# Performance work log

Measured on AMD Instinct MI355X. Metric: run time of the kernel, lower is better.

## Reference

```python
import jax, jax.numpy as jnp
import numpy as np

K_TOP = 8
TEMP = 0.1


def setup_inputs() -> dict:
    key = jax.random.key(0)
    k1, k2, k3, k4 = jax.random.split(key, 4)
    B, K, D, Db, C = 256, 64, 256, 512, 1024
    return {
        "slot_features": jax.random.normal(k1, (B, K, D), dtype=jnp.float32),
        "proj_W": jax.random.normal(k2, (D, Db), dtype=jnp.float32) * (1.0 / np.sqrt(D)),
        "proj_b": jax.random.normal(k3, (Db,), dtype=jnp.float32) * 0.01,
        "embed": jax.random.uniform(k4, (C, Db), dtype=jnp.float32),  # NMF atoms are nonnegative
    }


def reference(slot_features, proj_W, proj_b, embed):
    B, K, _ = slot_features.shape
    num_codes = embed.shape[0]

    # slot projection: [B, K, basis_dim]
    z_e = jnp.einsum('bkd,de->bke', slot_features, proj_W) + proj_b
    z_flat = z_e.reshape(B * K, -1)  # [N, Db]

    # Euclidean cdist via expanded squared norm (the GEMM is the heavy part)
    d2 = (jnp.sum(z_flat * z_flat, axis=-1, keepdims=True)
          + jnp.sum(embed * embed, axis=-1)[None, :]
          - 2.0 * (z_flat @ embed.T))  # [N, C]
    dist = jnp.sqrt(jnp.maximum(d2, 0.0))

    # top-k smallest distances
    neg_vals, indices_flat = jax.lax.top_k(-dist, K_TOP)  # [N, k]
    values = -neg_vals
    weights = jax.nn.softmax(-values / TEMP, axis=-1)  # [N, k]

    # gather atoms and interpolate
    selected_atoms = embed[indices_flat]  # [N, k, Db]
    q_flat = jnp.einsum('nk,nkd->nd', weights, selected_atoms)
    q_st = q_flat.reshape(B, K, -1)

    vq_loss = jnp.mean((z_e - jax.lax.stop_gradient(q_st)) ** 2)

    # average usage (equivalent to scatter into [N, C] then mean over N)
    avg_usage = jax.ops.segment_sum(weights.reshape(-1), indices_flat.reshape(-1),
                                    num_segments=num_codes) / (B * K)
    entropy = -jnp.sum(avg_usage * jnp.log(avg_usage + 1e-8))

    indices = indices_flat[:, 0].reshape(B, K)
    return q_st, indices, vq_loss, entropy
```

## Files before the change

### kernel.cpp

```cpp
#include <hip/hip_runtime.h>
#include <math.h>
#include <float.h>

#define NROWS  16384
#define DIN    256
#define DBASIS 512
#define CCODES 1024
#define KTOP   8
#define NCAND  16
#define TEMP_F 0.1f

typedef __attribute__((ext_vector_type(8))) short short8v;
typedef __attribute__((ext_vector_type(4))) float f32x4;

__device__ __forceinline__ unsigned short bf16_rne(float f) {
    unsigned int u = __float_as_uint(f);
    u += 0x7FFFu + ((u >> 16) & 1u);
    return (unsigned short)(u >> 16);
}
__device__ __forceinline__ float bf16_to_f32(unsigned short h) {
    return __uint_as_float(((unsigned int)h) << 16);
}

__global__ __launch_bounds__(256) void k_prep(const float* __restrict__ embed,
                                              unsigned short* __restrict__ Eh,
                                              unsigned short* __restrict__ El,
                                              float* __restrict__ en2,
                                              float* __restrict__ usage,
                                              float* __restrict__ vq_accum) {
    const int c = blockIdx.x * 256 + threadIdx.x;
    const float4* row = (const float4*)(embed + (size_t)c * DBASIS);
    ushort4* ehr = (ushort4*)(Eh + (size_t)c * DBASIS);
    ushort4* elr = (ushort4*)(El + (size_t)c * DBASIS);
    float s = 0.f;
    #pragma unroll 4
    for (int j = 0; j < DBASIS / 4; ++j) {
        const float4 v = row[j];
        s += v.x * v.x + v.y * v.y + v.z * v.z + v.w * v.w;
        ushort4 h, l;
        h.x = bf16_rne(v.x); l.x = bf16_rne(v.x - bf16_to_f32(h.x));
        h.y = bf16_rne(v.y); l.y = bf16_rne(v.y - bf16_to_f32(h.y));
        h.z = bf16_rne(v.z); l.z = bf16_rne(v.z - bf16_to_f32(h.z));
        h.w = bf16_rne(v.w); l.w = bf16_rne(v.w - bf16_to_f32(h.w));
        ehr[j] = h; elr[j] = l;
    }
    en2[c] = s;
    usage[c] = 0.f;
    if (c == 0) vq_accum[0] = 0.f;
}

__global__ __launch_bounds__(256, 2) void k_gemm_z(const float* __restrict__ A,
                                                   const float* __restrict__ Bm,
                                                   const float* __restrict__ bias,
                                                   float* __restrict__ Z,
                                                   unsigned short* __restrict__ Zh,
                                                   unsigned short* __restrict__ Zl) {
    __shared__ float As[16][132];
    __shared__ float Bs[16][132];
    const int tid = threadIdx.x;
    const int bm = blockIdx.x * 128;
    const int bn = blockIdx.y * 128;
    const int tx = tid & 15, ty = tid >> 4;
    float acc[2][2][4][4] = {};

    for (int k0 = 0; k0 < DIN; k0 += 16) {
        #pragma unroll
        for (int it = 0; it < 2; ++it) {
            const int r  = (tid >> 2) + it * 64;
            const int c4 = (tid & 3) * 4;
            const float4 a = *(const float4*)(A + (size_t)(bm + r) * DIN + k0 + c4);
            As[c4 + 0][r] = a.x; As[c4 + 1][r] = a.y;
            As[c4 + 2][r] = a.z; As[c4 + 3][r] = a.w;
        }
        {
            const int r  = tid >> 4;
            const int c8 = (tid & 15) * 8;
            const float4 b0 = *(const float4*)(Bm + (size_t)(k0 + r) * DBASIS + bn + c8);
            const float4 b1 = *(const float4*)(Bm + (size_t)(k0 + r) * DBASIS + bn + c8 + 4);
            *(float4*)&Bs[r][c8]     = b0;
            *(float4*)&Bs[r][c8 + 4] = b1;
        }
        __syncthreads();
        #pragma unroll
        for (int kk = 0; kk < 16; ++kk) {
            const float4 a0 = *(const float4*)&As[kk][ty * 4];
            const float4 a1 = *(const float4*)&As[kk][64 + ty * 4];
            const float4 b0 = *(const float4*)&Bs[kk][tx * 4];
            const float4 b1 = *(const float4*)&Bs[kk][64 + tx * 4];
            const float av[2][4] = {{a0.x, a0.y, a0.z, a0.w}, {a1.x, a1.y, a1.z, a1.w}};
            const float bv[2][4] = {{b0.x, b0.y, b0.z, b0.w}, {b1.x, b1.y, b1.z, b1.w}};
            #pragma unroll
            for (int qi = 0; qi < 2; ++qi)
                #pragma unroll
                for (int qj = 0; qj < 2; ++qj)
                    #pragma unroll
                    for (int i = 0; i < 4; ++i)
                        #pragma unroll
                        for (int j = 0; j < 4; ++j)
                            acc[qi][qj][i][j] = fmaf(av[qi][i], bv[qj][j], acc[qi][qj][i][j]);
        }
        __syncthreads();
    }
    #pragma unroll
    for (int qj = 0; qj < 2; ++qj) {
        const int colb = bn + qj * 64 + tx * 4;
        const float4 bv = *(const float4*)(bias + colb);
        const float bb[4] = {bv.x, bv.y, bv.z, bv.w};
        #pragma unroll
        for (int qi = 0; qi < 2; ++qi)
            #pragma unroll
            for (int i = 0; i < 4; ++i) {
                const int row = bm + qi * 64 + ty * 4 + i;
                float4 o;
                o.x = acc[qi][qj][i][0] + bb[0];
                o.y = acc[qi][qj][i][1] + bb[1];
                o.z = acc[qi][qj][i][2] + bb[2];
                o.w = acc[qi][qj][i][3] + bb[3];
                *(float4*)(Z + (size_t)row * DBASIS + colb) = o;
                ushort4 h, l;
                h.x = bf16_rne(o.x); l.x = bf16_rne(o.x - bf16_to_f32(h.x));
                h.y = bf16_rne(o.y); l.y = bf16_rne(o.y - bf16_to_f32(h.y));
                h.z = bf16_rne(o.z); l.z = bf16_rne(o.z - bf16_to_f32(h.z));
                h.w = bf16_rne(o.w); l.w = bf16_rne(o.w - bf16_to_f32(h.w));
                *(ushort4*)(Zh + (size_t)row * DBASIS + colb) = h;
                *(ushort4*)(Zl + (size_t)row * DBASIS + colb) = l;
            }
    }
}

__global__ __launch_bounds__(256, 2) void k_gemm_p(const unsigned short* __restrict__ Zh,
                                                   const unsigned short* __restrict__ Zl,
                                                   const unsigned short* __restrict__ Eh,
                                                   const unsigned short* __restrict__ El,
                                                   const float* __restrict__ en2,
                                                   float* __restrict__ P) {
    __shared__ __align__(16) short ldsA[4096];
    __shared__ __align__(16) short ldsB[4096];
    const int tid  = threadIdx.x;
    const int lane = tid & 63;
    const int w    = tid >> 6;
    const int wr   = w >> 1, wc = w & 1;
    const int bm   = blockIdx.x * 128;
    const int bc   = blockIdx.y * 128;

    f32x4 acc[4][4];
    #pragma unroll
    for (int i = 0; i < 4; ++i)
        #pragma unroll
        for (int j = 0; j < 4; ++j)
            acc[i][j] = (f32x4){0.f, 0.f, 0.f, 0.f};

    for (int ch = 0; ch < 48; ++ch) {
        const int term = ch >> 4;
        const int k0   = (ch & 15) * 32;
        const unsigned short* Asrc = (term == 2) ? Zl : Zh;
        const unsigned short* Bsrc = (term == 1) ? El : Eh;
        #pragma unroll
        for (int j = 0; j < 2; ++j) {
            const int gi = j * 256 + tid;
            const int g  = gi >> 7;
            const int r  = gi & 127;
            const unsigned short* ga = Asrc + (size_t)(bm + r) * DBASIS + k0 + g * 8;
            const unsigned short* gb = Bsrc + (size_t)(bc + r) * DBASIS + k0 + g * 8;
            __builtin_amdgcn_global_load_lds((const __attribute__((address_space(1))) void*)ga,
                                             (__attribute__((address_space(3))) void*)(&ldsA[gi * 8]),
                                             16, 0, 0);
            __builtin_amdgcn_global_load_lds((const __attribute__((address_space(1))) void*)gb,
                                             (__attribute__((address_space(3))) void*)(&ldsB[gi * 8]),
                                             16, 0, 0);
        }
        __syncthreads();

        const int kg = lane >> 4;
        const int lr = lane & 15;
        short8v af[4], bf[4];
        #pragma unroll
        for (int f = 0; f < 4; ++f) {
            af[f] = *(const short8v*)&ldsA[(kg * 128 + wr * 64 + f * 16 + lr) * 8];
            bf[f] = *(const short8v*)&ldsB[(kg * 128 + wc * 64 + f * 16 + lr) * 8];
        }
        #pragma unroll
        for (int fm = 0; fm < 4; ++fm)
            #pragma unroll
            for (int fn = 0; fn < 4; ++fn)
                acc[fm][fn] = __builtin_amdgcn_mfma_f32_16x16x32_bf16(af[fm], bf[fn], acc[fm][fn], 0, 0, 0);
        __syncthreads();
    }

    #pragma unroll
    for (int fn = 0; fn < 4; ++fn) {
        const int col = bc + wc * 64 + fn * 16 + (lane & 15);
        const float e2 = en2[col];
        #pragma unroll
        for (int fm = 0; fm < 4; ++fm) {
            const int row0 = bm + wr * 64 + fm * 16 + (lane >> 4) * 4;
            #pragma unroll
            for (int r = 0; r < 4; ++r)
                P[(size_t)(row0 + r) * CCODES + col] = e2 - 2.f * acc[fm][fn][r];
        }
    }
}

__global__ __launch_bounds__(256) void k_topk(const float* __restrict__ P,
                                              const float* __restrict__ Z,
                                              const float* __restrict__ embed,
                                              const float* __restrict__ en2,
                                              float* __restrict__ q_out,
                                              float* __restrict__ idx_out,
                                              float* __restrict__ usage,
                                              float* __restrict__ vq_accum) {
    const int tid  = threadIdx.x;
    const int lane = tid & 63;
    const int w    = tid >> 6;
    const int n    = blockIdx.x * 4 + w;

    float v[16];
    #pragma unroll
    for (int j = 0; j < 16; ++j) v[j] = P[(size_t)n * CCODES + lane + 64 * j];

    float zv[8];
    float zn2 = 0.f;
    #pragma unroll
    for (int j = 0; j < 8; ++j) {
        zv[j] = Z[(size_t)n * DBASIS + lane + 64 * j];
        zn2 = fmaf(zv[j], zv[j], zn2);
    }
    #pragma unroll
    for (int off = 32; off; off >>= 1) zn2 += __shfl_xor(zn2, off, 64);

    int idx16[NCAND];
    #pragma unroll
    for (int t = 0; t < NCAND; ++t) {
        float bv = v[0];
        int   bj = 0;
        #pragma unroll
        for (int j = 1; j < 16; ++j)
            if (v[j] < bv) { bv = v[j]; bj = j; }
        int bcn = lane + 64 * bj;
        #pragma unroll
        for (int off = 32; off; off >>= 1) {
            const float ov = __shfl_xor(bv, off, 64);
            const int   oc = __shfl_xor(bcn, off, 64);
            if (ov < bv || (ov == bv && oc < bcn)) { bv = ov; bcn = oc; }
        }
        idx16[t] = bcn;
        const int kl = bcn & 63, kj = bcn >> 6;
        #pragma unroll
        for (int j = 0; j < 16; ++j)
            if (lane == kl && j == kj) v[j] = FLT_MAX;
    }

    float d16[NCAND];
    #pragma unroll
    for (int t = 0; t < NCAND; ++t) {
        const int c = idx16[t];
        const float* er = embed + (size_t)c * DBASIS;
        float dot = 0.f;
        #pragma unroll
        for (int j = 0; j < 8; ++j) dot = fmaf(zv[j], er[lane + 64 * j], dot);
        #pragma unroll
        for (int off = 32; off; off >>= 1) dot += __shfl_xor(dot, off, 64);
        const float d2 = zn2 + en2[c] - 2.f * dot;
        d16[t] = sqrtf(fmaxf(d2, 0.f));
    }

    float dist[KTOP];
    int   idx[KTOP];
    #pragma unroll
    for (int t = 0; t < KTOP; ++t) {
        float bd = d16[0];
        int   bi = idx16[0];
        int   bu = 0;
        #pragma unroll
        for (int u = 1; u < NCAND; ++u) {
            const bool better = (d16[u] < bd) || (d16[u] == bd && idx16[u] < bi);
            if (better) { bd = d16[u]; bi = idx16[u]; bu = u; }
        }
        dist[t] = bd; idx[t] = bi;
        #pragma unroll
        for (int u = 0; u < NCAND; ++u)
            if (u == bu) d16[u] = FLT_MAX;
    }

    float wgt[KTOP];
    float s = 0.f;
    #pragma unroll
    for (int t = 0; t < KTOP; ++t) {
        wgt[t] = expf((dist[0] - dist[t]) * (1.0f / TEMP_F));
        s += wgt[t];
    }
    const float inv_s = 1.f / s;
    #pragma unroll
    for (int t = 0; t < KTOP; ++t) wgt[t] *= inv_s;

    float lloss = 0.f;
    #pragma unroll
    for (int j = 0; j < 8; ++j) {
        const int d = lane + 64 * j;
        float acc = 0.f;
        #pragma unroll
        for (int t = 0; t < KTOP; ++t)
            acc = fmaf(wgt[t], embed[(size_t)idx[t] * DBASIS + d], acc);
        q_out[(size_t)n * DBASIS + d] = acc;
        const float df = zv[j] - acc;
        lloss = fmaf(df, df, lloss);
    }
    #pragma unroll
    for (int off = 32; off; off >>= 1) lloss += __shfl_xor(lloss, off, 64);

    __shared__ float ls[4];
    if (lane == 0) ls[w] = lloss;
    __syncthreads();
    if (tid == 0) atomicAdd(vq_accum, ls[0] + ls[1] + ls[2] + ls[3]);

    #pragma unroll
    for (int t = 0; t < KTOP; ++t)
        if (lane == t) atomicAdd(usage + idx[t], wgt[t] * (1.0f / (float)NROWS));

    if (lane == 0) idx_out[n] = (float)idx[0];
}

__global__ __launch_bounds__(256) void k_final(const float* __restrict__ usage,
                                               const float* __restrict__ vq_accum,
                                               float* __restrict__ out_scalars) {
    __shared__ float red[256];
    float s = 0.f;
    for (int c = threadIdx.x; c < CCODES; c += 256) {
        const float u = usage[c];
        s += u * logf(u + 1e-8f);
    }
    red[threadIdx.x] = s;
    __syncthreads();
    for (int st = 128; st; st >>= 1) {
        if (threadIdx.x < st) red[threadIdx.x] += red[threadIdx.x + st];
        __syncthreads();
    }
    if (threadIdx.x == 0) {
        out_scalars[0] = vq_accum[0] * (1.0f / ((float)NROWS * (float)DBASIS));
        out_scalars[1] = -red[0];
    }
}

extern "C" void kernel_launch(void* const* d_in, const int* in_sizes, int n_in,
                              void* d_out, int out_size, void* d_ws, size_t ws_size,
                              hipStream_t stream) {
    const float* slot  = (const float*)d_in[0];
    const float* projW = (const float*)d_in[1];
    const float* projb = (const float*)d_in[2];
    const float* embed = (const float*)d_in[3];

    float* out  = (float*)d_out;
    float* q    = out;
    float* idxo = out + (size_t)NROWS * DBASIS;
    float* scal = idxo + NROWS;

    char* wsb = (char*)d_ws;
    float*          Z     = (float*)wsb;                                  wsb += (size_t)NROWS * DBASIS * 4;
    float*          P     = (float*)wsb;                                  wsb += (size_t)NROWS * CCODES * 4;
    unsigned short* Zh    = (unsigned short*)wsb;                         wsb += (size_t)NROWS * DBASIS * 2;
    unsigned short* Zl    = (unsigned short*)wsb;                         wsb += (size_t)NROWS * DBASIS * 2;
    unsigned short* Eh    = (unsigned short*)wsb;                         wsb += (size_t)CCODES * DBASIS * 2;
    unsigned short* El    = (unsigned short*)wsb;                         wsb += (size_t)CCODES * DBASIS * 2;
    float*          en2   = (float*)wsb;                                  wsb += CCODES * 4;
    float*          usage = (float*)wsb;                                  wsb += CCODES * 4;
    float*          vq    = (float*)wsb;

    k_prep<<<dim3(CCODES / 256), dim3(256), 0, stream>>>(embed, Eh, El, en2, usage, vq);
    k_gemm_z<<<dim3(NROWS / 128, DBASIS / 128), dim3(256), 0, stream>>>(slot, projW, projb, Z, Zh, Zl);
    k_gemm_p<<<dim3(NROWS / 128, CCODES / 128), dim3(256), 0, stream>>>(Zh, Zl, Eh, El, en2, P);
    k_topk<<<dim3(NROWS / 4), dim3(256), 0, stream>>>(P, Z, embed, en2, q, idxo, usage, vq);
    k_final<<<dim3(1), dim3(256), 0, stream>>>(usage, vq, scal);
}
```

Before: 411.1 us.

## Move projection GEMM to split-bf16 MFMA and use ballot threshold top-k selection

Replaces the fp32 SIMT projection GEMM with a three-term bf16 MFMA GEMM (hi*hi, hi*lo, lo*hi). Two new prep kernels split the slot features and the transposed weights into high and low bf16 parts. The top-k kernel now packs distance and code index into a 32-bit key. A ballot-driven binary search finds a threshold that admits at least 16 candidates, which are compacted into LDS and rescored exactly in fp32. This drops the 16 serial wave-wide argmin passes but adds extra prep traffic and a data-dependent number of candidates to rescore.

```diff
diff --git a/kernel.cpp b/kernel.cpp
--- a/kernel.cpp
+++ b/kernel.cpp
@@ -7,7 +7,6 @@
 #define DBASIS 512
 #define CCODES 1024
 #define KTOP   8
-#define NCAND  16
 #define TEMP_F 0.1f
 
 typedef __attribute__((ext_vector_type(8))) short short8v;
@@ -20,6 +19,10 @@
 }
 __device__ __forceinline__ float bf16_to_f32(unsigned short h) {
     return __uint_as_float(((unsigned int)h) << 16);
+}
+__device__ __forceinline__ unsigned packkey(float p, float zn2, unsigned cidx) {
+    const float d2 = fmaxf(p + zn2, 0.f);
+    return (__float_as_uint(d2) & 0xFFFFFC00u) | cidx;
 }
 
 __global__ __launch_bounds__(256) void k_prep(const float* __restrict__ embed,
@@ -49,82 +52,119 @@
     if (c == 0) vq_accum[0] = 0.f;
 }
 
-__global__ __launch_bounds__(256, 2) void k_gemm_z(const float* __restrict__ A,
-                                                   const float* __restrict__ Bm,
-                                                   const float* __restrict__ bias,
-                                                   float* __restrict__ Z,
-                                                   unsigned short* __restrict__ Zh,
-                                                   unsigned short* __restrict__ Zl) {
-    __shared__ float As[16][132];
-    __shared__ float Bs[16][132];
-    const int tid = threadIdx.x;
-    const int bm = blockIdx.x * 128;
-    const int bn = blockIdx.y * 128;
-    const int tx = tid & 15, ty = tid >> 4;
-    float acc[2][2][4][4] = {};
-
-    for (int k0 = 0; k0 < DIN; k0 += 16) {
-        #pragma unroll
-        for (int it = 0; it < 2; ++it) {
-            const int r  = (tid >> 2) + it * 64;
-            const int c4 = (tid & 3) * 4;
-            const float4 a = *(const float4*)(A + (size_t)(bm + r) * DIN + k0 + c4);
-            As[c4 + 0][r] = a.x; As[c4 + 1][r] = a.y;
-            As[c4 + 2][r] = a.z; As[c4 + 3][r] = a.w;
-        }
-        {
-            const int r  = tid >> 4;
-            const int c8 = (tid & 15) * 8;
-            const float4 b0 = *(const float4*)(Bm + (size_t)(k0 + r) * DBASIS + bn + c8);
-            const float4 b1 = *(const float4*)(Bm + (size_t)(k0 + r) * DBASIS + bn + c8 + 4);
-            *(float4*)&Bs[r][c8]     = b0;
-            *(float4*)&Bs[r][c8 + 4] = b1;
+__global__ __launch_bounds__(256) void k_prep_slot(const float* __restrict__ in,
+                                                   unsigned short* __restrict__ Sh,
+                                                   unsigned short* __restrict__ Sl) {
+    const int i = blockIdx.x * 256 + threadIdx.x;
+    const float4 v = ((const float4*)in)[i];
+    ushort4 h, l;
+    h.x = bf16_rne(v.x); l.x = bf16_rne(v.x - bf16_to_f32(h.x));
+    h.y = bf16_rne(v.y); l.y = bf16_rne(v.y - bf16_to_f32(h.y));
+    h.z = bf16_rne(v.z); l.z = bf16_rne(v.z - bf16_to_f32(h.z));
+    h.w = bf16_rne(v.w); l.w = bf16_rne(v.w - bf16_to_f32(h.w));
+    ((ushort4*)Sh)[i] = h;
+    ((ushort4*)Sl)[i] = l;
+}
+
+__global__ __launch_bounds__(256) void k_prep_w(const float* __restrict__ W,
+                                                unsigned short* __restrict__ Wh,
+                                                unsigned short* __restrict__ Wl) {
+    __shared__ float tile[32][33];
+    const int k0 = blockIdx.x * 32;
+    const int n0 = blockIdx.y * 32;
+    const int tx = threadIdx.x & 31, ty = threadIdx.x >> 5;
+    #pragma unroll
+    for (int i = 0; i < 32; i += 8)
+        tile[ty + i][tx] = W[(size_t)(k0 + ty + i) * DBASIS + n0 + tx];
+    __syncthreads();
+    #pragma unroll
+    for (int i = 0; i < 32; i += 8) {
+        const int n = n0 + ty + i, k = k0 + tx;
+        const float v = tile[tx][ty + i];
+        const unsigned short h = bf16_rne(v);
+        Wh[(size_t)n * DIN + k] = h;
+        Wl[(size_t)n * DIN + k] = bf16_rne(v - bf16_to_f32(h));
+    }
+}
+
+__global__ __launch_bounds__(256, 2) void k_gemm_z_mfma(const unsigned short* __restrict__ Sh,
+                                                        const unsigned short* __restrict__ Sl,
+                                                        const unsigned short* __restrict__ Wh,
+                                                        const unsigned short* __restrict__ Wl,
+                                                        const float* __restrict__ bias,
+                                                        float* __restrict__ Z,
+                                                        unsigned short* __restrict__ Zh,
+                                                        unsigned short* __restrict__ Zl) {
+    __shared__ __align__(16) short ldsA[4096];
+    __shared__ __align__(16) short ldsB[4096];
+    const int tid  = threadIdx.x;
+    const int lane = tid & 63;
+    const int w    = tid >> 6;
+    const int wr   = w >> 1, wc = w & 1;
+    const int bm   = blockIdx.x * 128;
+    const int bc   = blockIdx.y * 128;
+
+    f32x4 acc[4][4];
+    #pragma unroll
+    for (int i = 0; i < 4; ++i)
+        #pragma unroll
+        for (int j = 0; j < 4; ++j)
+            acc[i][j] = (f32x4){0.f, 0.f, 0.f, 0.f};
+
+    for (int ch = 0; ch < 24; ++ch) {
+        const int term = ch >> 3;
+        const int k0   = (ch & 7) * 32;
+        const unsigned short* Asrc = (term == 2) ? Sl : Sh;
+        const unsigned short* Bsrc = (term == 1) ? Wl : Wh;
+        #pragma unroll
+        for (int j = 0; j < 2; ++j) {
+            const int gi = j * 256 + tid;
+            const int g  = gi >> 7;
+            const int r  = gi & 127;
+            const unsigned short* ga = Asrc + (size_t)(bm + r) * DIN + k0 + g * 8;
+            const unsigned short* gb = Bsrc + (size_t)(bc + r) * DIN + k0 + g * 8;
+            __builtin_amdgcn_global_load_lds((const __attribute__((address_space(1))) void*)ga,
+                                             (__attribute__((address_space(3))) void*)(&ldsA[gi * 8]),
+                                             16, 0, 0);
+            __builtin_amdgcn_global_load_lds((const __attribute__((address_space(1))) void*)gb,
+                                             (__attribute__((address_space(3))) void*)(&ldsB[gi * 8]),
+                                             16, 0, 0);
         }
         __syncthreads();
-        #pragma unroll
-        for (int kk = 0; kk < 16; ++kk) {
-            const float4 a0 = *(const float4*)&As[kk][ty * 4];
-            const float4 a1 = *(const float4*)&As[kk][64 + ty * 4];
-            const float4 b0 = *(const float4*)&Bs[kk][tx * 4];
-            const float4 b1 = *(const float4*)&Bs[kk][64 + tx * 4];
-            const float av[2][4] = {{a0.x, a0.y, a0.z, a0.w}, {a1.x, a1.y, a1.z, a1.w}};
-            const float bv[2][4] = {{b0.x, b0.y, b0.z, b0.w}, {b1.x, b1.y, b1.z, b1.w}};
+
+        const int kg = lane >> 4;
+        const int lr = lane & 15;
+        short8v af[4], bf[4];
+        #pragma unroll
+        for (int f = 0; f < 4; ++f) {
+            af[f] = *(const short8v*)&ldsA[(kg * 128 + wr * 64 + f * 16 + lr) * 8];
+            bf[f] = *(const short8v*)&ldsB[(kg * 128 + wc * 64 + f * 16 + lr) * 8];
+        }
+        #pragma unroll
+        for (int fm = 0; fm < 4; ++fm)
             #pragma unroll
-            for (int qi = 0; qi < 2; ++qi)
-                #pragma unroll
-                for (int qj = 0; qj < 2; ++qj)
-                    #pragma unroll
-                    for (int i = 0; i < 4; ++i)
-                        #pragma unroll
-                        for (int j = 0; j < 4; ++j)
-                            acc[qi][qj][i][j] = fmaf(av[qi][i], bv[qj][j], acc[qi][qj][i][j]);
-        }
+            for (int fn = 0; fn < 4; ++fn)
+                acc[fm][fn] = __builtin_amdgcn_mfma_f32_16x16x32_bf16(af[fm], bf[fn], acc[fm][fn], 0, 0, 0);
         __syncthreads();
     }
-    #pragma unroll
-    for (int qj = 0; qj < 2; ++qj) {
-        const int colb = bn + qj * 64 + tx * 4;
-        const float4 bv = *(const float4*)(bias + colb);
-        const float bb[4] = {bv.x, bv.y, bv.z, bv.w};
-        #pragma unroll
-        for (int qi = 0; qi < 2; ++qi)
+
+    #pragma unroll
+    for (int fn = 0; fn < 4; ++fn) {
+        const int col = bc + wc * 64 + fn * 16 + (lane & 15);
+        const float bb = bias[col];
+        #pragma unroll
+        for (int fm = 0; fm < 4; ++fm) {
+            const int row0 = bm + wr * 64 + fm * 16 + (lane >> 4) * 4;
             #pragma unroll
-            for (int i = 0; i < 4; ++i) {
-                const int row = bm + qi * 64 + ty * 4 + i;
-                float4 o;
-                o.x = acc[qi][qj][i][0] + bb[0];
-                o.y = acc[qi][qj][i][1] + bb[1];
-                o.z = acc[qi][qj][i][2] + bb[2];
-                o.w = acc[qi][qj][i][3] + bb[3];
-                *(float4*)(Z + (size_t)row * DBASIS + colb) = o;
-                ushort4 h, l;
-                h.x = bf16_rne(o.x); l.x = bf16_rne(o.x - bf16_to_f32(h.x));
-                h.y = bf16_rne(o.y); l.y = bf16_rne(o.y - bf16_to_f32(h.y));
-                h.z = bf16_rne(o.z); l.z = bf16_rne(o.z - bf16_to_f32(h.z));
-                h.w = bf16_rne(o.w); l.w = bf16_rne(o.w - bf16_to_f32(h.w));
-                *(ushort4*)(Zh + (size_t)row * DBASIS + colb) = h;
-                *(ushort4*)(Zl + (size_t)row * DBASIS + colb) = l;
+            for (int r = 0; r < 4; ++r) {
+                const float val = acc[fm][fn][r] + bb;
+                const size_t o = (size_t)(row0 + r) * DBASIS + col;
+                Z[o] = val;
+                const unsigned short h = bf16_rne(val);
+                Zh[o] = h;
+                Zl[o] = bf16_rne(val - bf16_to_f32(h));
             }
+        }
     }
 }
 
@@ -214,9 +254,8 @@
     const int w    = tid >> 6;
     const int n    = blockIdx.x * 4 + w;
 
-    float v[16];
-    #pragma unroll
-    for (int j = 0; j < 16; ++j) v[j] = P[(size_t)n * CCODES + lane + 64 * j];
+    __shared__ int   cand_lds[4][64];
+    __shared__ float ls[4];
 
     float zv[8];
     float zn2 = 0.f;
@@ -228,58 +267,70 @@
     #pragma unroll
     for (int off = 32; off; off >>= 1) zn2 += __shfl_xor(zn2, off, 64);
 
-    int idx16[NCAND];
-    #pragma unroll
-    for (int t = 0; t < NCAND; ++t) {
-        float bv = v[0];
-        int   bj = 0;
-        #pragma unroll
-        for (int j = 1; j < 16; ++j)
-            if (v[j] < bv) { bv = v[j]; bj = j; }
-        int bcn = lane + 64 * bj;
+    const float4* prow = (const float4*)(P + (size_t)n * CCODES + lane * 16);
+    const unsigned cbase = (unsigned)(lane * 16);
+    unsigned key[16];
+    #pragma unroll
+    for (int j = 0; j < 4; ++j) {
+        const float4 v = prow[j];
+        key[4 * j + 0] = packkey(v.x, zn2, cbase + 4 * j + 0);
+        key[4 * j + 1] = packkey(v.y, zn2, cbase + 4 * j + 1);
+        key[4 * j + 2] = packkey(v.z, zn2, cbase + 4 * j + 2);
+        key[4 * j + 3] = packkey(v.w, zn2, cbase + 4 * j + 3);
+    }
+
+    unsigned kmin = key[0];
+    #pragma unroll
+    for (int t = 1; t < 16; ++t) kmin = (key[t] < kmin) ? key[t] : kmin;
+
+    unsigned lo = 0u, hi = 0xFFFFFFFFu;
+    while (lo < hi) {
+        const unsigned mid = lo + ((hi - lo) >> 1);
+        const unsigned long long mk = __ballot(kmin <= mid);
+        if (__popcll(mk) >= 16) hi = mid; else lo = mid + 1;
+    }
+    const unsigned T = lo;
+
+    int* clist = cand_lds[w];
+    int base = 0;
+    #pragma unroll
+    for (int t = 0; t < 16; ++t) {
+        const bool pred = (key[t] <= T);
+        const unsigned long long mk = __ballot(pred);
+        const int pos = base + __popcll(mk & ((1ull << lane) - 1ull));
+        if (pred && pos < 64) clist[pos] = (int)(cbase + t);
+        base += __popcll(mk);
+    }
+    const int m = base < 64 ? base : 64;
+
+    float mydist = FLT_MAX;
+    int   myidx  = 0x7FFFFFFF;
+    for (int t = 0; t < m; ++t) {
+        const int c = clist[t];
+        const float* er = embed + (size_t)c * DBASIS;
+        float dot = 0.f;
+        #pragma unroll
+        for (int j = 0; j < 8; ++j) dot = fmaf(zv[j], er[lane + 64 * j], dot);
+        #pragma unroll
+        for (int off = 32; off; off >>= 1) dot += __shfl_xor(dot, off, 64);
+        const float d = sqrtf(fmaxf(zn2 + en2[c] - 2.f * dot, 0.f));
+        if (lane == t) { mydist = d; myidx = c; }
+    }
+
+    float dist[KTOP];
+    int   idx[KTOP];
+    #pragma unroll
+    for (int p = 0; p < KTOP; ++p) {
+        float bv = mydist;
+        int   bi = myidx;
         #pragma unroll
         for (int off = 32; off; off >>= 1) {
             const float ov = __shfl_xor(bv, off, 64);
-            const int   oc = __shfl_xor(bcn, off, 64);
-            if (ov < bv || (ov == bv && oc < bcn)) { bv = ov; bcn = oc; }
-        }
-        idx16[t] = bcn;
-        const int kl = bcn & 63, kj = bcn >> 6;
-        #pragma unroll
-        for (int j = 0; j < 16; ++j)
-            if (lane == kl && j == kj) v[j] = FLT_MAX;
-    }
-
-    float d16[NCAND];
-    #pragma unroll
-    for (int t = 0; t < NCAND; ++t) {
-        const int c = idx16[t];
-        const float* er = embed + (size_t)c * DBASIS;
-        float dot = 0.f;
-        #pragma unroll
-        for (int j = 0; j < 8; ++j) dot = fmaf(zv[j], er[lane + 64 * j], dot);
-        #pragma unroll
-        for (int off = 32; off; off >>= 1) dot += __shfl_xor(dot, off, 64);
-        const float d2 = zn2 + en2[c] - 2.f * dot;
-        d16[t] = sqrtf(fmaxf(d2, 0.f));
-    }
-
-    float dist[KTOP];
-    int   idx[KTOP];
-    #pragma unroll
-    for (int t = 0; t < KTOP; ++t) {
-        float bd = d16[0];
-        int   bi = idx16[0];
-        int   bu = 0;
-        #pragma unroll
-        for (int u = 1; u < NCAND; ++u) {
-            const bool better = (d16[u] < bd) || (d16[u] == bd && idx16[u] < bi);
-            if (better) { bd = d16[u]; bi = idx16[u]; bu = u; }
-        }
-        dist[t] = bd; idx[t] = bi;
-        #pragma unroll
-        for (int u = 0; u < NCAND; ++u)
-            if (u == bu) d16[u] = FLT_MAX;
+            const int   oi = __shfl_xor(bi, off, 64);
+            if (ov < bv || (ov == bv && oi < bi)) { bv = ov; bi = oi; }
+        }
+        dist[p] = bv; idx[p] = bi;
+        if (myidx == bi) { mydist = FLT_MAX; myidx = 0x7FFFFFFF; }
     }
 
     float wgt[KTOP];
@@ -308,7 +359,6 @@
     #pragma unroll
     for (int off = 32; off; off >>= 1) lloss += __shfl_xor(lloss, off, 64);
 
-    __shared__ float ls[4];
     if (lane == 0) ls[w] = lloss;
     __syncthreads();
     if (tid == 0) atomicAdd(vq_accum, ls[0] + ls[1] + ls[2] + ls[3]);
@@ -355,18 +405,24 @@
     float* scal = idxo + NROWS;
 
     char* wsb = (char*)d_ws;
-    float*          Z     = (float*)wsb;                                  wsb += (size_t)NROWS * DBASIS * 4;
-    float*          P     = (float*)wsb;                                  wsb += (size_t)NROWS * CCODES * 4;
-    unsigned short* Zh    = (unsigned short*)wsb;                         wsb += (size_t)NROWS * DBASIS * 2;
-    unsigned short* Zl    = (unsigned short*)wsb;                         wsb += (size_t)NROWS * DBASIS * 2;
-    unsigned short* Eh    = (unsigned short*)wsb;                         wsb += (size_t)CCODES * DBASIS * 2;
-    unsigned short* El    = (unsigned short*)wsb;                         wsb += (size_t)CCODES * DBASIS * 2;
-    float*          en2   = (float*)wsb;                                  wsb += CCODES * 4;
-    float*          usage = (float*)wsb;                                  wsb += CCODES * 4;
+    float*          Z     = (float*)wsb;          wsb += (size_t)NROWS * DBASIS * 4;
+    float*          P     = (float*)wsb;          wsb += (size_t)NROWS * CCODES * 4;
+    unsigned short* Zh    = (unsigned short*)wsb; wsb += (size_t)NROWS * DBASIS * 2;
+    unsigned short* Zl    = (unsigned short*)wsb; wsb += (size_t)NROWS * DBASIS * 2;
+    unsigned short* Eh    = (unsigned short*)wsb; wsb += (size_t)CCODES * DBASIS * 2;
+    unsigned short* El    = (unsigned short*)wsb; wsb += (size_t)CCODES * DBASIS * 2;
+    unsigned short* Sh    = (unsigned short*)wsb; wsb += (size_t)NROWS * DIN * 2;
+    unsigned short* Sl    = (unsigned short*)wsb; wsb += (size_t)NROWS * DIN * 2;
+    unsigned short* Wh    = (unsigned short*)wsb; wsb += (size_t)DBASIS * DIN * 2;
+    unsigned short* Wl    = (unsigned short*)wsb; wsb += (size_t)DBASIS * DIN * 2;
+    float*          en2   = (float*)wsb;          wsb += CCODES * 4;
+    float*          usage = (float*)wsb;          wsb += CCODES * 4;
     float*          vq    = (float*)wsb;
 
     k_prep<<<dim3(CCODES / 256), dim3(256), 0, stream>>>(embed, Eh, El, en2, usage, vq);
-    k_gemm_z<<<dim3(NROWS / 128, DBASIS / 128), dim3(256), 0, stream>>>(slot, projW, projb, Z, Zh, Zl);
+    k_prep_slot<<<dim3(NROWS * DIN / 4 / 256), dim3(256), 0, stream>>>(slot, Sh, Sl);
+    k_prep_w<<<dim3(DIN / 32, DBASIS / 32), dim3(256), 0, stream>>>(projW, Wh, Wl);
+    k_gemm_z_mfma<<<dim3(NROWS / 128, DBASIS / 128), dim3(256), 0, stream>>>(Sh, Sl, Wh, Wl, projb, Z, Zh, Zl);
     k_gemm_p<<<dim3(NROWS / 128, CCODES / 128), dim3(256), 0, stream>>>(Zh, Zl, Eh, El, en2, P);
     k_topk<<<dim3(NROWS / 4), dim3(256), 0, stream>>>(P, Z, embed, en2, q, idxo, usage, vq);
     k_final<<<dim3(1), dim3(256), 0, stream>>>(usage, vq, scal);
```

Result: faster. 380.6 us (-7.4%).

## Double-buffer split-bf16 GEMM and use threshold-based candidate selection in top-k

Applied to the files above, without the earlier changes.

The distance GEMM now stages all four bf16 hi/lo tiles at once into a double-buffered LDS region. It issues the three MFMA products per k-chunk, prefetching the next chunk while computing the current one, and swaps the grid axes so neighbouring blocks share Z rows. The top-k kernel replaces 16 serial wave-wide argmin passes with packed distance/index keys and a ballot-based binary search for a threshold that keeps at least 16 candidates. The candidates are compacted into LDS and exact fp32 distances are recomputed for up to 64 of them. This raises LDS usage to 64KB per block, which may reduce occupancy, and caps candidates at 64 when there are ties.

```diff
diff --git a/kernel.cpp b/kernel.cpp
--- a/kernel.cpp
+++ b/kernel.cpp
@@ -7,7 +7,6 @@
 #define DBASIS 512
 #define CCODES 1024
 #define KTOP   8
-#define NCAND  16
 #define TEMP_F 0.1f
 
 typedef __attribute__((ext_vector_type(8))) short short8v;
@@ -21,6 +20,14 @@
 __device__ __forceinline__ float bf16_to_f32(unsigned short h) {
     return __uint_as_float(((unsigned int)h) << 16);
 }
+__device__ __forceinline__ unsigned packkey(float p, float zn2, unsigned cidx) {
+    const float d2 = fmaxf(p + zn2, 0.f);
+    return (__float_as_uint(d2) & 0xFFFFFC00u) | cidx;
+}
+
+#define GLOAD16(gsrc, ldst) \
+    __builtin_amdgcn_global_load_lds((const __attribute__((address_space(1))) void*)(gsrc), \
+                                     (__attribute__((address_space(3))) void*)(ldst), 16, 0, 0)
 
 __global__ __launch_bounds__(256) void k_prep(const float* __restrict__ embed,
                                               unsigned short* __restrict__ Eh,
@@ -134,14 +141,15 @@
                                                    const unsigned short* __restrict__ El,
                                                    const float* __restrict__ en2,
                                                    float* __restrict__ P) {
-    __shared__ __align__(16) short ldsA[4096];
-    __shared__ __align__(16) short ldsB[4096];
+    __shared__ __align__(16) short lds[2][4][4096];
     const int tid  = threadIdx.x;
     const int lane = tid & 63;
     const int w    = tid >> 6;
     const int wr   = w >> 1, wc = w & 1;
-    const int bm   = blockIdx.x * 128;
-    const int bc   = blockIdx.y * 128;
+    const int bm   = blockIdx.y * 128;
+    const int bc   = blockIdx.x * 128;
+    const int kg   = lane >> 4;
+    const int lr   = lane & 15;
 
     f32x4 acc[4][4];
     #pragma unroll
@@ -150,46 +158,56 @@
         for (int j = 0; j < 4; ++j)
             acc[i][j] = (f32x4){0.f, 0.f, 0.f, 0.f};
 
-    for (int ch = 0; ch < 48; ++ch) {
-        const int term = ch >> 4;
-        const int k0   = (ch & 15) * 32;
-        const unsigned short* Asrc = (term == 2) ? Zl : Zh;
-        const unsigned short* Bsrc = (term == 1) ? El : Eh;
-        #pragma unroll
-        for (int j = 0; j < 2; ++j) {
-            const int gi = j * 256 + tid;
-            const int g  = gi >> 7;
-            const int r  = gi & 127;
-            const unsigned short* ga = Asrc + (size_t)(bm + r) * DBASIS + k0 + g * 8;
-            const unsigned short* gb = Bsrc + (size_t)(bc + r) * DBASIS + k0 + g * 8;
-            __builtin_amdgcn_global_load_lds((const __attribute__((address_space(1))) void*)ga,
-                                             (__attribute__((address_space(3))) void*)(&ldsA[gi * 8]),
-                                             16, 0, 0);
-            __builtin_amdgcn_global_load_lds((const __attribute__((address_space(1))) void*)gb,
-                                             (__attribute__((address_space(3))) void*)(&ldsB[gi * 8]),
-                                             16, 0, 0);
-        }
+#define STAGE_P(BUF, PH) do {                                                  \
+        const int k0_ = (PH) * 32;                                             \
+        _Pragma("unroll")                                                      \
+        for (int j_ = 0; j_ < 2; ++j_) {                                       \
+            const int gi_ = j_ * 256 + tid;                                    \
+            const int g_  = gi_ >> 7, r_ = gi_ & 127;                          \
+            const size_t ao_ = (size_t)(bm + r_) * DBASIS + k0_ + g_ * 8;      \
+            const size_t bo_ = (size_t)(bc + r_) * DBASIS + k0_ + g_ * 8;      \
+            GLOAD16(Zh + ao_, &lds[BUF][0][gi_ * 8]);                          \
+            GLOAD16(Zl + ao_, &lds[BUF][1][gi_ * 8]);                          \
+            GLOAD16(Eh + bo_, &lds[BUF][2][gi_ * 8]);                          \
+            GLOAD16(El + bo_, &lds[BUF][3][gi_ * 8]);                          \
+        }                                                                      \
+    } while (0)
+
+#define COMPUTE_P(BUF) do {                                                    \
+        short8v afh[4], afl[4], bfh[4], bfl[4];                                \
+        _Pragma("unroll")                                                      \
+        for (int f = 0; f < 4; ++f) {                                          \
+            const int ai = (kg * 128 + wr * 64 + f * 16 + lr) * 8;             \
+            const int bi = (kg * 128 + wc * 64 + f * 16 + lr) * 8;             \
+            afh[f] = *(const short8v*)&lds[BUF][0][ai];                        \
+            afl[f] = *(const short8v*)&lds[BUF][1][ai];                        \
+            bfh[f] = *(const short8v*)&lds[BUF][2][bi];                        \
+            bfl[f] = *(const short8v*)&lds[BUF][3][bi];                        \
+        }                                                                      \
+        _Pragma("unroll")                                                      \
+        for (int fm = 0; fm < 4; ++fm)                                         \
+            _Pragma("unroll")                                                  \
+            for (int fn = 0; fn < 4; ++fn) {                                   \
+                acc[fm][fn] = __builtin_amdgcn_mfma_f32_16x16x32_bf16(afh[fm], bfh[fn], acc[fm][fn], 0, 0, 0); \
+                acc[fm][fn] = __builtin_amdgcn_mfma_f32_16x16x32_bf16(afh[fm], bfl[fn], acc[fm][fn], 0, 0, 0); \
+                acc[fm][fn] = __builtin_amdgcn_mfma_f32_16x16x32_bf16(afl[fm], bfh[fn], acc[fm][fn], 0, 0, 0); \
+            }                                                                  \
+    } while (0)
+
+    STAGE_P(0, 0);
+    __syncthreads();
+    int cur = 0;
+    for (int ph = 0; ph < 15; ++ph) {
+        STAGE_P(cur ^ 1, ph + 1);
+        COMPUTE_P(cur);
         __syncthreads();
-
-        const int kg = lane >> 4;
-        const int lr = lane & 15;
-        short8v af[4], bf[4];
-        #pragma unroll
-        for (int f = 0; f < 4; ++f) {
-            af[f] = *(const short8v*)&ldsA[(kg * 128 + wr * 64 + f * 16 + lr) * 8];
-            bf[f] = *(const short8v*)&ldsB[(kg * 128 + wc * 64 + f * 16 + lr) * 8];
-        }
-        #pragma unroll
-        for (int fm = 0; fm < 4; ++fm)
-            #pragma unroll
-            for (int fn = 0; fn < 4; ++fn)
-                acc[fm][fn] = __builtin_amdgcn_mfma_f32_16x16x32_bf16(af[fm], bf[fn], acc[fm][fn], 0, 0, 0);
-        __syncthreads();
-    }
+        cur ^= 1;
+    }
+    COMPUTE_P(cur);
 
     #pragma unroll
     for (int fn = 0; fn < 4; ++fn) {
-        const int col = bc + wc * 64 + fn * 16 + (lane & 15);
+        const int col = bc + wc * 64 + fn * 16 + lr;
         const float e2 = en2[col];
         #pragma unroll
         for (int fm = 0; fm < 4; ++fm) {
@@ -199,6 +217,8 @@
                 P[(size_t)(row0 + r) * CCODES + col] = e2 - 2.f * acc[fm][fn][r];
         }
     }
+#undef STAGE_P
+#undef COMPUTE_P
 }
 
 __global__ __launch_bounds__(256) void k_topk(const float* __restrict__ P,
@@ -214,9 +234,8 @@
     const int w    = tid >> 6;
     const int n    = blockIdx.x * 4 + w;
 
-    float v[16];
-    #pragma unroll
-    for (int j = 0; j < 16; ++j) v[j] = P[(size_t)n * CCODES + lane + 64 * j];
+    __shared__ int   cand_lds[4][64];
+    __shared__ float ls[4];
 
     float zv[8];
     float zn2 = 0.f;
@@ -228,58 +247,70 @@
     #pragma unroll
     for (int off = 32; off; off >>= 1) zn2 += __shfl_xor(zn2, off, 64);
 
-    int idx16[NCAND];
-    #pragma unroll
-    for (int t = 0; t < NCAND; ++t) {
-        float bv = v[0];
-        int   bj = 0;
-        #pragma unroll
-        for (int j = 1; j < 16; ++j)
-            if (v[j] < bv) { bv = v[j]; bj = j; }
-        int bcn = lane + 64 * bj;
+    const float4* prow = (const float4*)(P + (size_t)n * CCODES + lane * 16);
+    const unsigned cbase = (unsigned)(lane * 16);
+    unsigned key[16];
+    #pragma unroll
+    for (int j = 0; j < 4; ++j) {
+        const float4 v = prow[j];
+        key[4 * j + 0] = packkey(v.x, zn2, cbase + 4 * j + 0);
+        key[4 * j + 1] = packkey(v.y, zn2, cbase + 4 * j + 1);
+        key[4 * j + 2] = packkey(v.z, zn2, cbase + 4 * j + 2);
+        key[4 * j + 3] = packkey(v.w, zn2, cbase + 4 * j + 3);
+    }
+
+    unsigned kmin = key[0];
+    #pragma unroll
+    for (int t = 1; t < 16; ++t) kmin = (key[t] < kmin) ? key[t] : kmin;
+
+    unsigned lo = 0u, hi = 0xFFFFFFFFu;
+    while (lo < hi) {
+        const unsigned mid = lo + ((hi - lo) >> 1);
+        const unsigned long long mk = __ballot(kmin <= mid);
+        if (__popcll(mk) >= 16) hi = mid; else lo = mid + 1;
+    }
+    const unsigned T = lo;
+
+    int* clist = cand_lds[w];
+    int base = 0;
+    #pragma unroll
+    for (int t = 0; t < 16; ++t) {
+        const bool pred = (key[t] <= T);
+        const unsigned long long mk = __ballot(pred);
+        const int pos = base + __popcll(mk & ((1ull << lane) - 1ull));
+        if (pred && pos < 64) clist[pos] = (int)(cbase + t);
+        base += __popcll(mk);
+    }
+    const int m = base < 64 ? base : 64;
+
+    float mydist = FLT_MAX;
+    int   myidx  = 0x7FFFFFFF;
+    for (int t = 0; t < m; ++t) {
+        const int c = clist[t];
+        const float* er = embed + (size_t)c * DBASIS;
+        float dot = 0.f;
+        #pragma unroll
+        for (int j = 0; j < 8; ++j) dot = fmaf(zv[j], er[lane + 64 * j], dot);
+        #pragma unroll
+        for (int off = 32; off; off >>= 1) dot += __shfl_xor(dot, off, 64);
+        const float d = sqrtf(fmaxf(zn2 + en2[c] - 2.f * dot, 0.f));
+        if (lane == t) { mydist = d; myidx = c; }
+    }
+
+    float dist[KTOP];
+    int   idx[KTOP];
+    #pragma unroll
+    for (int p = 0; p < KTOP; ++p) {
+        float bv = mydist;
+        int   bi = myidx;
         #pragma unroll
         for (int off = 32; off; off >>= 1) {
             const float ov = __shfl_xor(bv, off, 64);
-            const int   oc = __shfl_xor(bcn, off, 64);
-            if (ov < bv || (ov == bv && oc < bcn)) { bv = ov; bcn = oc; }
+            const int   oi = __shfl_xor(bi, off, 64);
+            if (ov < bv || (ov == bv && oi < bi)) { bv = ov; bi = oi; }
         }
-        idx16[t] = bcn;
-        const int kl = bcn & 63, kj = bcn >> 6;
-        #pragma unroll
-        for (int j = 0; j < 16; ++j)
-            if (lane == kl && j == kj) v[j] = FLT_MAX;
-    }
-
-    float d16[NCAND];
-    #pragma unroll
-    for (int t = 0; t < NCAND; ++t) {
-        const int c = idx16[t];
-        const float* er = embed + (size_t)c * DBASIS;
-        float dot = 0.f;
-        #pragma unroll
-        for (int j = 0; j < 8; ++j) dot = fmaf(zv[j], er[lane + 64 * j], dot);
-        #pragma unroll
-        for (int off = 32; off; off >>= 1) dot += __shfl_xor(dot, off, 64);
-        const float d2 = zn2 + en2[c] - 2.f * dot;
-        d16[t] = sqrtf(fmaxf(d2, 0.f));
-    }
-
-    float dist[KTOP];
-    int   idx[KTOP];
-    #pragma unroll
-    for (int t = 0; t < KTOP; ++t) {
-        float bd = d16[0];
-        int   bi = idx16[0];
-        int   bu = 0;
-        #pragma unroll
-        for (int u = 1; u < NCAND; ++u) {
-            const bool better = (d16[u] < bd) || (d16[u] == bd && idx16[u] < bi);
-            if (better) { bd = d16[u]; bi = idx16[u]; bu = u; }
-        }
-        dist[t] = bd; idx[t] = bi;
-        #pragma unroll
-        for (int u = 0; u < NCAND; ++u)
-            if (u == bu) d16[u] = FLT_MAX;
+        dist[p] = bv; idx[p] = bi;
+        if (myidx == bi) { mydist = FLT_MAX; myidx = 0x7FFFFFFF; }
     }
 
     float wgt[KTOP];
@@ -308,7 +339,6 @@
     #pragma unroll
     for (int off = 32; off; off >>= 1) lloss += __shfl_xor(lloss, off, 64);
 
-    __shared__ float ls[4];
     if (lane == 0) ls[w] = lloss;
     __syncthreads();
     if (tid == 0) atomicAdd(vq_accum, ls[0] + ls[1] + ls[2] + ls[3]);
@@ -355,19 +385,19 @@
     float* scal = idxo + NROWS;
 
     char* wsb = (char*)d_ws;
-    float*          Z     = (float*)wsb;                                  wsb += (size_t)NROWS * DBASIS * 4;
-    float*          P     = (float*)wsb;                                  wsb += (size_t)NROWS * CCODES * 4;
-    unsigned short* Zh    = (unsigned short*)wsb;                         wsb += (size_t)NROWS * DBASIS * 2;
-    unsigned short* Zl    = (unsigned short*)wsb;                         wsb += (size_t)NROWS * DBASIS * 2;
-    unsigned short* Eh    = (unsigned short*)wsb;                         wsb += (size_t)CCODES * DBASIS * 2;
-    unsigned short* El    = (unsigned short*)wsb;                         wsb += (size_t)CCODES * DBASIS * 2;
-    float*          en2   = (float*)wsb;                                  wsb += CCODES * 4;
-    float*          usage = (float*)wsb;                                  wsb += CCODES * 4;
+    float*          Z     = (float*)wsb;          wsb += (size_t)NROWS * DBASIS * 4;
+    float*          P     = (float*)wsb;          wsb += (size_t)NROWS * CCODES * 4;
+    unsigned short* Zh    = (unsigned short*)wsb; wsb += (size_t)NROWS * DBASIS * 2;
+    unsigned short* Zl    = (unsigned short*)wsb; wsb += (size_t)NROWS * DBASIS * 2;
+    unsigned short* Eh    = (unsigned short*)wsb; wsb += (size_t)CCODES * DBASIS * 2;
+    unsigned short* El    = (unsigned short*)wsb; wsb += (size_t)CCODES * DBASIS * 2;
+    float*          en2   = (float*)wsb;          wsb += CCODES * 4;
+    float*          usage = (float*)wsb;          wsb += CCODES * 4;
     float*          vq    = (float*)wsb;
 
     k_prep<<<dim3(CCODES / 256), dim3(256), 0, stream>>>(embed, Eh, El, en2, usage, vq);
     k_gemm_z<<<dim3(NROWS / 128, DBASIS / 128), dim3(256), 0, stream>>>(slot, projW, projb, Z, Zh, Zl);
-    k_gemm_p<<<dim3(NROWS / 128, CCODES / 128), dim3(256), 0, stream>>>(Zh, Zl, Eh, El, en2, P);
+    k_gemm_p<<<dim3(CCODES / 128, NROWS / 128), dim3(256), 0, stream>>>(Zh, Zl, Eh, El, en2, P);
     k_topk<<<dim3(NROWS / 4), dim3(256), 0, stream>>>(P, Z, embed, en2, q, idxo, usage, vq);
     k_final<<<dim3(1), dim3(256), 0, stream>>>(usage, vq, scal);
 }
```

New measurement: 371.9 us. 1.11x faster.
